# Kernel optimization log

Hardware: AMD Instinct MI355X
Metric: run time of the kernel (lower is better)

The kernel has to match this reference:

```python
import jax, jax.numpy as jnp
import numpy as np

SR = 3            # search_range
K = 5             # template_sz
S = 2 * SR + 1    # search window size (7)
KSZ = 5           # bilateral kernel size
SIG_S = 1.5       # bilateral spatial sigma
SIG_I = 0.05      # bilateral intensity sigma


def _patches(x, k, pad):
    # x: (B,C,H,W) -> (B, C*k*k, H', W'); channel order (C, kh, kw) matches torch unfold
    return jax.lax.conv_general_dilated_patches(x, (k, k), (1, 1), pad)


def _binomial(x):
    # separable [1 2 1]/4 with replicate padding
    xp = jnp.pad(x, ((0, 0), (0, 0), (1, 1), (0, 0)), mode='edge')
    v = (xp[:, :, :-2, :] + 2.0 * x + xp[:, :, 2:, :]) / 4.0
    vp = jnp.pad(v, ((0, 0), (0, 0), (0, 0), (1, 1)), mode='edge')
    return (vp[:, :, :, :-2] + 2.0 * v + vp[:, :, :, 2:]) / 4.0


def _gradient(f):
    fp = jnp.pad(f, ((0, 0), (0, 0), (1, 1), (1, 1)), mode='edge')
    fy = (fp[:, :, 2:, 1:-1] - fp[:, :, :-2, 1:-1]) / 2.0
    fx = (fp[:, :, 1:-1, 2:] - fp[:, :, 1:-1, :-2]) / 2.0
    return fy, fx


def _templates(img):
    # (B,1,H,W) -> (B,H,W,1,K*K)  per-pixel KxK patch (zero SAME padding)
    p = _patches(img, K, [(K // 2, K // 2)] * 2)      # (B,K*K,H,W)
    return jnp.transpose(p, (0, 2, 3, 1))[:, :, :, None, :]


def _search_windows(img):
    # (B,1,H,W) -> (B,H,W,S*S,K*K): KxK templates at every displacement in SxS window
    B, _, H, W = img.shape
    xp = jnp.pad(img, ((0, 0), (0, 0), (SR, SR), (SR, SR)))      # zero pad by max_sr
    p1 = _patches(xp, K, [(K // 2, K // 2)] * 2)                  # (B,K*K,H+2SR,W+2SR)
    p2 = _patches(p1, S, 'VALID')                                 # (B,K*K*S*S,H,W)
    p2 = p2.reshape(B, K * K, S, S, H, W)
    return jnp.transpose(p2, (0, 4, 5, 2, 3, 1)).reshape(B, H, W, S * S, K * K)


def _spiral_rank():
    # rank of each flat (S*S) displacement in a center-out spiral traversal
    sz = S
    order = np.zeros(sz * sz, np.int32)
    j = i = 0
    rank = 0
    order[(j + SR) * sz + (i + SR)] = rank
    rank += 1
    dirs = [(0, 1), (1, 0), (0, -1), (-1, 0)]
    d, step = 0, 1
    while rank < sz * sz:
        for _ in range(2):
            dj, di = dirs[d % 4]
            for _ in range(step):
                j += dj
                i += di
                if abs(j) <= SR and abs(i) <= SR and rank < sz * sz:
                    order[(j + SR) * sz + (i + SR)] = rank
                    rank += 1
            d += 1
        step += 1
    return jnp.asarray(order)


def _subpixel(f_t, g_t, f_img):
    # f_t, g_t: (B,H,W,1,K*K) in 0..255; f_img: (B,1,H,W) float in [0,1]
    f = f_t / 255.0
    g = g_t / 255.0
    dfy_img, dfx_img = _gradient(f_img)
    dfy = _templates(dfy_img)
    dfx = _templates(dfx_img)
    pm = np.zeros((K, K), np.float32)
    pm[0, :] = pm[-1, :] = pm[:, 0] = pm[:, -1] = 1.0   # border ring mask
    pred = jnp.asarray(pm.reshape(-1))
    rs = lambda x: jnp.sum(x, axis=-1, keepdims=True)
    a = rs(dfx * dfx * pred)
    b = rs(dfx * dfy * pred)
    d = rs(dfy * dfy * pred)
    z = g - f
    p = rs(z * dfx * pred)
    q = rs(z * dfy * pred)
    det = a * d - b * b
    u = d * p - b * q
    v = a * q - b * p
    sub = jnp.concatenate([v, u], axis=-1)              # (B,H,W,1,2) (y,x)
    det_bad = det <= 1e-7
    sub = sub / jnp.where(det_bad, 1.0, det)            # safe divide; masked anyway
    sub = jnp.where(det_bad | (jnp.abs(sub) >= 1.0), 0.0, sub)
    return jnp.transpose(sub[:, :, :, 0, :], (0, 3, 1, 2))   # (B,2,H,W)


def _median3(x):
    # 3x3 median with replicate (SYMMETRIC) padding
    B, C, H, W = x.shape
    xp = jnp.pad(x, ((0, 0), (0, 0), (1, 1), (1, 1)), mode='edge')
    p = _patches(xp, 3, 'VALID').reshape(B, C, 9, H, W)
    return jnp.sort(p, axis=2)[:, :, 4]


def _bilateral(t, vec):
    # t: (B,1,H,W) guide; vec: (B,2,H,W) flow
    B, _, H, W = t.shape
    k2 = KSZ * KSZ
    kernel = -1.0 / (2.0 * SIG_S ** 2) * jnp.ones((k2,), jnp.float32)
    sii = 1.0 / (2.0 * SIG_I ** 2)
    cp = jnp.transpose(t, (0, 2, 3, 1))[:, :, :, None, :]                # (B,H,W,1,1)
    ck = jnp.transpose(_patches(t, KSZ, [(KSZ // 2, KSZ // 2)] * 2).reshape(B, 1, k2, H, W), (0, 3, 4, 2, 1))  # (B,H,W,k2,1)
    idiff = jnp.sum((cp - ck) ** 2, axis=-1)                             # (B,H,W,k2)
    coeff = jnp.clip(1.0 - jnp.abs(kernel - idiff * sii), 0.0, 1.0)[..., None]
    vb = jnp.transpose(_patches(vec, KSZ, [(KSZ // 2, KSZ // 2)] * 2).reshape(B, 2, k2, H, W), (0, 3, 4, 2, 1))  # (B,H,W,k2,2)
    out = jnp.sum(vb * coeff, axis=-2) / jnp.sum(coeff, axis=-2)
    return jnp.transpose(out, (0, 3, 1, 2))


def setup_inputs() -> dict:
    key = jax.random.key(0)
    k1, k2 = jax.random.split(key)
    H = W = 256
    f_img = jax.random.uniform(k1, (1, 1, H, W), jnp.float32)
    g_img = jax.random.uniform(k2, (1, 1, H, W), jnp.float32)
    return {'f_img': f_img, 'g_img': g_img}


def reference(f_img, g_img):
    fb = _binomial(f_img)
    gb = _binomial(g_img)
    # quantize to uint8-valued floats (matches _cast float->uint8)
    fq = jnp.clip(jnp.round(fb * 255.0), 0.0, 255.0)
    gq = jnp.clip(jnp.round(gb * 255.0), 0.0, 255.0)
    w1 = _search_windows(fq)                 # (B,H,W,S*S,K*K)
    w2 = _templates(gq)                      # (B,H,W,1,K*K)
    cost = jnp.sum(jnp.abs(w1 - w2), axis=-1).astype(jnp.int32)   # (B,H,W,S*S)
    rank = _spiral_rank()
    score = cost * 64 + rank                 # lexicographic (cost, spiral rank); rank < 64
    idx = jnp.argmin(score, axis=-1)         # (B,H,W) spiral-centered argmin
    rng = jnp.arange(-SR, SR + 1, dtype=jnp.float32)
    jj, ii = jnp.meshgrid(rng, rng, indexing='ij')
    vecLUT = -jnp.stack([jj, ii], axis=-1).reshape(-1, 2)
    vector = jnp.transpose(vecLUT[idx], (0, 3, 1, 2))             # (B,2,H,W)
    min_t = jnp.take_along_axis(w1, idx[:, :, :, None, None], axis=3)  # (B,H,W,1,K*K)
    sub = _subpixel(min_t, w2, fb)
    flow = vector + sub
    flow = _median3(flow)
    flow = _bilateral(fb, flow)
    return flow
```

## Files before the change

### kernel.cpp

```cpp
#include <hip/hip_runtime.h>
#include <math.h>

#define H 256
#define W 256
#define TS 16

#if __has_builtin(__builtin_amdgcn_alignbyte)
__device__ __forceinline__ unsigned align_b(unsigned hi, unsigned lo, int sh) {
    return __builtin_amdgcn_alignbyte(hi, lo, sh);
}
#else
__device__ __forceinline__ unsigned align_b(unsigned hi, unsigned lo, int sh) {
    unsigned d;
    asm("v_alignbyte_b32 %0, %1, %2, %3" : "=v"(d) : "v"(hi), "v"(lo), "v"(sh));
    return d;
}
#endif

#if __has_builtin(__builtin_amdgcn_sad_u8)
__device__ __forceinline__ unsigned sad_u8(unsigned a, unsigned b, unsigned acc) {
    return __builtin_amdgcn_sad_u8(a, b, acc);
}
#else
__device__ __forceinline__ unsigned sad_u8(unsigned a, unsigned b, unsigned acc) {
    unsigned d;
    asm("v_sad_u8 %0, %1, %2, %3" : "=v"(d) : "v"(a), "v"(b), "v"(acc));
    return d;
}
#endif

__device__ __forceinline__ float binom3x3(const float* s, int r, int c, int stride) {
    float vm = (s[(r-1)*stride + (c-1)] + 2.0f*s[r*stride + (c-1)] + s[(r+1)*stride + (c-1)]) * 0.25f;
    float v0 = (s[(r-1)*stride + (c  )] + 2.0f*s[r*stride + (c  )] + s[(r+1)*stride + (c  )]) * 0.25f;
    float vp = (s[(r-1)*stride + (c+1)] + 2.0f*s[r*stride + (c+1)] + s[(r+1)*stride + (c+1)]) * 0.25f;
    return (vm + 2.0f*v0 + vp) * 0.25f;
}

__device__ __forceinline__ unsigned quant255(float v) {
    return (unsigned)fminf(fmaxf(rintf(v * 255.0f), 0.0f), 255.0f);
}

__global__ void __launch_bounds__(256)
k_flow_fused(const float* __restrict__ f, const float* __restrict__ g,
             float* __restrict__ out) {
    __shared__ float    sf[36 * 36];
    __shared__ float    sg[28 * 28];
    __shared__ float    sfb[34 * 35];
    __shared__ unsigned sfq[34 * 9];
    __shared__ unsigned sgq[26 * 7];
    __shared__ float    sflow[2][22 * 22];
    __shared__ float    smed[2][20 * 20];

    int tx = threadIdx.x, ty = threadIdx.y;
    int bx0 = blockIdx.x * TS, by0 = blockIdx.y * TS;
    int tid = ty * TS + tx;

    for (int i = tid; i < 36 * 36; i += 256) {
        int r = i / 36, c = i % 36;
        int gy = min(max(by0 + r - 10, 0), H - 1);
        int gx = min(max(bx0 + c - 10, 0), W - 1);
        sf[i] = f[gy * W + gx];
    }
    for (int i = tid; i < 28 * 28; i += 256) {
        int r = i / 28, c = i % 28;
        int gy = min(max(by0 + r - 6, 0), H - 1);
        int gx = min(max(bx0 + c - 6, 0), W - 1);
        sg[i] = g[gy * W + gx];
    }
    __syncthreads();

    for (int i = tid; i < 306 + 182; i += 256) {
        if (i < 306) {
            int row = i / 9, dw = i % 9;
            unsigned pack = 0;
            #pragma unroll
            for (int b = 0; b < 4; b++) {
                int col = dw * 4 + b;
                unsigned q = 0;
                if (col < 34) {
                    float bv = 0.0f;
                    int gy = by0 + row - 9, gx = bx0 + col - 9;
                    if (gy >= 0 && gy < H && gx >= 0 && gx < W) {
                        bv = binom3x3(sf, row + 1, col + 1, 36);
                        q = quant255(bv);
                    }
                    sfb[row * 35 + col] = bv;
                }
                pack |= q << (8 * b);
            }
            sfq[i] = pack;
        } else {
            int j = i - 306;
            int row = j / 7, dw = j % 7;
            unsigned pack = 0;
            #pragma unroll
            for (int b = 0; b < 4; b++) {
                int col = dw * 4 + b;
                unsigned q = 0;
                if (col < 26) {
                    int gy = by0 + row - 5, gx = bx0 + col - 5;
                    if (gy >= 0 && gy < H && gx >= 0 && gx < W)
                        q = quant255(binom3x3(sg, row + 1, col + 1, 28));
                }
                pack |= q << (8 * b);
            }
            sgq[j] = pack;
        }
    }
    __syncthreads();

    const unsigned char* sfq_b = (const unsigned char*)sfq;

    const unsigned RANKC[49] = {
        42,43,44,45,46,47,48,
        41,20,21,22,23,24,25,
        40,19, 6, 7, 8, 9,26,
        39,18, 5, 0, 1,10,27,
        38,17, 4, 3, 2,11,28,
        37,16,15,14,13,12,29,
        36,35,34,33,32,31,30
    };

    for (int it = tid; it < 22 * 22; it += 256) {
        int r = it / 22, c = it % 22;
        int py = min(max(by0 + r - 3, 0), H - 1);
        int px = min(max(bx0 + c - 3, 0), W - 1);
        int ro = py - by0 + 9, co = px - bx0 + 9;
        int base = (co - 5) >> 2, a = (co - 5) & 3;

        unsigned w0[11], w1[11], w2[11];
        #pragma unroll
        for (int r2 = 0; r2 < 11; r2++) {
            const unsigned* row = &sfq[(ro - 5 + r2) * 9 + base];
            unsigned d0 = row[0], d1 = row[1], d2 = row[2], d3 = row[3];
            w0[r2] = align_b(d1, d0, a);
            w1[r2] = align_b(d2, d1, a);
            w2[r2] = align_b(d3, d2, a);
        }

        int gro = py - by0 + 5, gco = px - bx0 + 5;
        int gbase = (gco - 2) >> 2, ga = (gco - 2) & 3;
        unsigned gt_lo[5], gt_hi[5];
        #pragma unroll
        for (int kh = 0; kh < 5; kh++) {
            const unsigned* row = &sgq[(gro - 2 + kh) * 7 + gbase];
            unsigned d0 = row[0], d1 = row[1];
            gt_lo[kh] = align_b(d1, d0, ga);
            gt_hi[kh] = (d1 >> (8 * ga)) & 0xFFu;
        }

        unsigned best = 0xFFFFFFFFu;
        int bestd = 0;
        #pragma unroll
        for (int si = 0; si < 7; si++) {
            unsigned fd[11], f5[11];
            #pragma unroll
            for (int r2 = 0; r2 < 11; r2++) {
                fd[r2] = (si < 4) ? align_b(w1[r2], w0[r2], si) : align_b(w2[r2], w1[r2], si - 4);
                f5[r2] = (si < 4) ? ((w1[r2] >> (8 * si)) & 0xFFu)
                                  : ((w2[r2] >> (8 * (si - 4))) & 0xFFu);
            }
            #pragma unroll
            for (int sj = 0; sj < 7; sj++) {
                unsigned acc0 = 0, acc1 = 0;
                #pragma unroll
                for (int kh = 0; kh < 5; kh++) {
                    acc0 = sad_u8(fd[sj + kh], gt_lo[kh], acc0);
                    acc1 = sad_u8(f5[sj + kh], gt_hi[kh], acc1);
                }
                unsigned score = ((acc0 + acc1) << 6) + RANKC[sj * 7 + si];
                if (score < best) { best = score; bestd = sj * 7 + si; }
            }
        }
        int dy = bestd / 7 - 3, dx = bestd % 7 - 3;

        float aA = 0.f, bB = 0.f, dD = 0.f, pP = 0.f, qQ = 0.f;
        #pragma unroll
        for (int kh = 0; kh < 5; kh++) {
            #pragma unroll
            for (int kw = 0; kw < 5; kw++) {
                if (kh != 0 && kh != 4 && kw != 0 && kw != 4) continue;
                int yy = py + kh - 2, xx = px + kw - 2;
                if (yy < 0 || yy >= H || xx < 0 || xx >= W) continue;
                int fy = yy - by0 + 9;
                int fx = xx - bx0 + 9;
                int xl = max(xx - 1, 0) - bx0 + 9, xr = min(xx + 1, W - 1) - bx0 + 9;
                int yu = max(yy - 1, 0) - by0 + 9, yd = min(yy + 1, H - 1) - by0 + 9;
                float gxv = (sfb[fy * 35 + xr] - sfb[fy * 35 + xl]) * 0.5f;
                float gyv = (sfb[yd * 35 + fx] - sfb[yu * 35 + fx]) * 0.5f;
                float fv = (float)sfq_b[(ro + dy + kh - 2) * 36 + (co + dx + kw - 2)] * (1.0f / 255.0f);
                float gv = (float)((kw < 4) ? ((gt_lo[kh] >> (8 * kw)) & 0xFFu) : gt_hi[kh]) * (1.0f / 255.0f);
                float z = gv - fv;
                aA += gxv * gxv;
                bB += gxv * gyv;
                dD += gyv * gyv;
                pP += z * gxv;
                qQ += z * gyv;
            }
        }
        float det = aA * dD - bB * bB;
        float u = dD * pP - bB * qQ;
        float v = aA * qQ - bB * pP;
        float suby = 0.f, subx = 0.f;
        if (det > 1e-7f) {
            suby = v / det;
            subx = u / det;
            if (fabsf(suby) >= 1.0f) suby = 0.f;
            if (fabsf(subx) >= 1.0f) subx = 0.f;
        }
        sflow[0][it] = (float)(-dy) + suby;
        sflow[1][it] = (float)(-dx) + subx;
    }
    __syncthreads();

    for (int i = tid; i < 2 * 20 * 20; i += 256) {
        int ch = i / 400, rem = i % 400;
        int rm = rem / 20, cm = rem % 20;
        int my = by0 + rm - 2, mx = bx0 + cm - 2;
        float m = 0.0f;
        if (my >= 0 && my < H && mx >= 0 && mx < W) {
            float v[9];
            int n = 0;
            #pragma unroll
            for (int dj = -1; dj <= 1; dj++) {
                #pragma unroll
                for (int di = -1; di <= 1; di++) {
                    int fr = min(max(my + dj, 0), H - 1) - by0 + 3;
                    int fc = min(max(mx + di, 0), W - 1) - bx0 + 3;
                    v[n++] = sflow[ch][fr * 22 + fc];
                }
            }
#define MSWAP(A, B) { float t_ = fminf(v[A], v[B]); v[B] = fmaxf(v[A], v[B]); v[A] = t_; }
            MSWAP(1,2); MSWAP(4,5); MSWAP(7,8);
            MSWAP(0,1); MSWAP(3,4); MSWAP(6,7);
            MSWAP(1,2); MSWAP(4,5); MSWAP(7,8);
            MSWAP(0,3); MSWAP(5,8); MSWAP(4,7);
            MSWAP(3,6); MSWAP(1,4); MSWAP(2,5);
            MSWAP(4,7); MSWAP(4,2); MSWAP(6,4);
            MSWAP(4,2);
#undef MSWAP
            m = v[4];
        }
        smed[ch][i % 400] = m;
    }
    __syncthreads();

    int x = bx0 + tx, y = by0 + ty;
    const float kern = -0.22222222222222221f;
    const float sii  = 200.0f;
    float cp = sfb[(ty + 9) * 35 + (tx + 9)];
    float sc = 0.f, sy = 0.f, sx = 0.f;
    #pragma unroll
    for (int j = 0; j < 5; j++) {
        #pragma unroll
        for (int i = 0; i < 5; i++) {
            float ck = sfb[(ty + 7 + j) * 35 + (tx + 7 + i)];
            float df = cp - ck;
            float coeff = 1.0f - fabsf(kern - df * df * sii);
            coeff = fminf(fmaxf(coeff, 0.0f), 1.0f);
            int s = (ty + j) * 20 + (tx + i);
            sc += coeff;
            sy += coeff * smed[0][s];
            sx += coeff * smed[1][s];
        }
    }
    out[y * W + x]         = sy / sc;
    out[H * W + y * W + x] = sx / sc;
}

extern "C" void kernel_launch(void* const* d_in, const int* in_sizes, int n_in,
                              void* d_out, int out_size, void* d_ws, size_t ws_size,
                              hipStream_t stream) {
    const float* f = (const float*)d_in[0];
    const float* g = (const float*)d_in[1];
    float* out = (float*)d_out;
    (void)d_ws; (void)ws_size;

    dim3 blk(TS, TS);
    dim3 grd(W / TS, H / TS);
    k_flow_fused<<<grd, blk, 0, stream>>>(f, g, out);
}
```

Baseline: 67.99 us.

## Split block-matching search across thread pairs with 512-thread blocks

```diff
diff --git a/kernel.cpp b/kernel.cpp
--- a/kernel.cpp
+++ b/kernel.cpp
@@ -40,7 +40,7 @@
     return (unsigned)fminf(fmaxf(rintf(v * 255.0f), 0.0f), 255.0f);
 }
 
-__global__ void __launch_bounds__(256)
+__global__ void __launch_bounds__(512)
 k_flow_fused(const float* __restrict__ f, const float* __restrict__ g,
              float* __restrict__ out) {
     __shared__ float    sf[36 * 36];
@@ -51,17 +51,16 @@
     __shared__ float    sflow[2][22 * 22];
     __shared__ float    smed[2][20 * 20];
 
-    int tx = threadIdx.x, ty = threadIdx.y;
     int bx0 = blockIdx.x * TS, by0 = blockIdx.y * TS;
-    int tid = ty * TS + tx;
-
-    for (int i = tid; i < 36 * 36; i += 256) {
+    int tid = threadIdx.x;
+
+    for (int i = tid; i < 36 * 36; i += 512) {
         int r = i / 36, c = i % 36;
         int gy = min(max(by0 + r - 10, 0), H - 1);
         int gx = min(max(bx0 + c - 10, 0), W - 1);
         sf[i] = f[gy * W + gx];
     }
-    for (int i = tid; i < 28 * 28; i += 256) {
+    for (int i = tid; i < 28 * 28; i += 512) {
         int r = i / 28, c = i % 28;
         int gy = min(max(by0 + r - 6, 0), H - 1);
         int gx = min(max(bx0 + c - 6, 0), W - 1);
@@ -69,7 +68,8 @@
     }
     __syncthreads();
 
-    for (int i = tid; i < 306 + 182; i += 256) {
+    if (tid < 306 + 182) {
+        int i = tid;
         if (i < 306) {
             int row = i / 9, dw = i % 9;
             unsigned pack = 0;
@@ -121,21 +121,21 @@
         36,35,34,33,32,31,30
     };
 
-    for (int it = tid; it < 22 * 22; it += 256) {
+    for (int u = tid; u < 2 * 22 * 22; u += 512) {
+        int it = u >> 1, half = u & 1;
         int r = it / 22, c = it % 22;
         int py = min(max(by0 + r - 3, 0), H - 1);
         int px = min(max(bx0 + c - 3, 0), W - 1);
         int ro = py - by0 + 9, co = px - bx0 + 9;
         int base = (co - 5) >> 2, a = (co - 5) & 3;
 
-        unsigned w0[11], w1[11], w2[11];
+        unsigned wA[11], wB[11];
         #pragma unroll
         for (int r2 = 0; r2 < 11; r2++) {
-            const unsigned* row = &sfq[(ro - 5 + r2) * 9 + base];
-            unsigned d0 = row[0], d1 = row[1], d2 = row[2], d3 = row[3];
-            w0[r2] = align_b(d1, d0, a);
-            w1[r2] = align_b(d2, d1, a);
-            w2[r2] = align_b(d3, d2, a);
+            const unsigned* row = &sfq[(ro - 5 + r2) * 9 + base + half];
+            unsigned dA = row[0], dB = row[1], dC = row[2];
+            wA[r2] = align_b(dB, dA, a);
+            wB[r2] = align_b(dC, dB, a);
         }
 
         int gro = py - by0 + 5, gco = px - bx0 + 5;
@@ -152,26 +152,34 @@
         unsigned best = 0xFFFFFFFFu;
         int bestd = 0;
         #pragma unroll
-        for (int si = 0; si < 7; si++) {
-            unsigned fd[11], f5[11];
-            #pragma unroll
-            for (int r2 = 0; r2 < 11; r2++) {
-                fd[r2] = (si < 4) ? align_b(w1[r2], w0[r2], si) : align_b(w2[r2], w1[r2], si - 4);
-                f5[r2] = (si < 4) ? ((w1[r2] >> (8 * si)) & 0xFFu)
-                                  : ((w2[r2] >> (8 * (si - 4))) & 0xFFu);
-            }
-            #pragma unroll
-            for (int sj = 0; sj < 7; sj++) {
-                unsigned acc0 = 0, acc1 = 0;
+        for (int sl = 0; sl < 4; sl++) {
+            if (!(sl == 3 && half)) {
+                unsigned fd[11], f5[11];
                 #pragma unroll
-                for (int kh = 0; kh < 5; kh++) {
-                    acc0 = sad_u8(fd[sj + kh], gt_lo[kh], acc0);
-                    acc1 = sad_u8(f5[sj + kh], gt_hi[kh], acc1);
-                }
-                unsigned score = ((acc0 + acc1) << 6) + RANKC[sj * 7 + si];
-                if (score < best) { best = score; bestd = sj * 7 + si; }
-            }
-        }
+                for (int r2 = 0; r2 < 11; r2++) {
+                    fd[r2] = align_b(wB[r2], wA[r2], sl);
+                    f5[r2] = (wB[r2] >> (8 * sl)) & 0xFFu;
+                }
+                #pragma unroll
+                for (int sj = 0; sj < 7; sj++) {
+                    unsigned acc0 = 0, acc1 = 0;
+                    #pragma unroll
+                    for (int kh = 0; kh < 5; kh++) {
+                        acc0 = sad_u8(fd[sj + kh], gt_lo[kh], acc0);
+                        acc1 = sad_u8(f5[sj + kh], gt_hi[kh], acc1);
+                    }
+                    int i0 = sj * 7 + sl;
+                    int i1 = sj * 7 + 4 + sl; if (i1 > 48) i1 = 48;
+                    unsigned rk = half ? RANKC[i1] : RANKC[i0];
+                    unsigned score = ((acc0 + acc1) << 6) + rk;
+                    int dsp = sj * 7 + sl + (half << 2);
+                    if (score < best) { best = score; bestd = dsp; }
+                }
+            }
+        }
+        unsigned obest = __shfl_xor(best, 1);
+        int obestd = __shfl_xor(bestd, 1);
+        if (obest < best) { best = obest; bestd = obestd; }
         int dy = bestd / 7 - 3, dx = bestd % 7 - 3;
 
         float aA = 0.f, bB = 0.f, dD = 0.f, pP = 0.f, qQ = 0.f;
@@ -199,21 +207,23 @@
             }
         }
         float det = aA * dD - bB * bB;
-        float u = dD * pP - bB * qQ;
-        float v = aA * qQ - bB * pP;
+        float u2 = dD * pP - bB * qQ;
+        float v2 = aA * qQ - bB * pP;
         float suby = 0.f, subx = 0.f;
         if (det > 1e-7f) {
-            suby = v / det;
-            subx = u / det;
+            suby = v2 / det;
+            subx = u2 / det;
             if (fabsf(suby) >= 1.0f) suby = 0.f;
             if (fabsf(subx) >= 1.0f) subx = 0.f;
         }
-        sflow[0][it] = (float)(-dy) + suby;
-        sflow[1][it] = (float)(-dx) + subx;
-    }
-    __syncthreads();
-
-    for (int i = tid; i < 2 * 20 * 20; i += 256) {
+        if (!half) {
+            sflow[0][it] = (float)(-dy) + suby;
+            sflow[1][it] = (float)(-dx) + subx;
+        }
+    }
+    __syncthreads();
+
+    for (int i = tid; i < 2 * 20 * 20; i += 512) {
         int ch = i / 400, rem = i % 400;
         int rm = rem / 20, cm = rem % 20;
         int my = by0 + rm - 2, mx = bx0 + cm - 2;
@@ -241,31 +251,32 @@
 #undef MSWAP
             m = v[4];
         }
-        smed[ch][i % 400] = m;
-    }
-    __syncthreads();
-
-    int x = bx0 + tx, y = by0 + ty;
-    const float kern = -0.22222222222222221f;
-    const float sii  = 200.0f;
-    float cp = sfb[(ty + 9) * 35 + (tx + 9)];
-    float sc = 0.f, sy = 0.f, sx = 0.f;
-    #pragma unroll
-    for (int j = 0; j < 5; j++) {
-        #pragma unroll
-        for (int i = 0; i < 5; i++) {
-            float ck = sfb[(ty + 7 + j) * 35 + (tx + 7 + i)];
-            float df = cp - ck;
-            float coeff = 1.0f - fabsf(kern - df * df * sii);
-            coeff = fminf(fmaxf(coeff, 0.0f), 1.0f);
-            int s = (ty + j) * 20 + (tx + i);
-            sc += coeff;
-            sy += coeff * smed[0][s];
-            sx += coeff * smed[1][s];
-        }
-    }
-    out[y * W + x]         = sy / sc;
-    out[H * W + y * W + x] = sx / sc;
+        smed[ch][rem] = m;
+    }
+    __syncthreads();
+
+    {
+        int ch = tid >> 8, pix = tid & 255;
+        int tx = pix & 15, ty = pix >> 4;
+        int x = bx0 + tx, y = by0 + ty;
+        const float kern = -0.22222222222222221f;
+        const float sii  = 200.0f;
+        float cp = sfb[(ty + 9) * 35 + (tx + 9)];
+        float sc = 0.f, sv = 0.f;
+        #pragma unroll
+        for (int j = 0; j < 5; j++) {
+            #pragma unroll
+            for (int i = 0; i < 5; i++) {
+                float ck = sfb[(ty + 7 + j) * 35 + (tx + 7 + i)];
+                float df = cp - ck;
+                float coeff = 1.0f - fabsf(kern - df * df * sii);
+                coeff = fminf(fmaxf(coeff, 0.0f), 1.0f);
+                sc += coeff;
+                sv += coeff * smed[ch][(ty + j) * 20 + (tx + i)];
+            }
+        }
+        out[ch * H * W + y * W + x] = sv / sc;
+    }
 }
 
 extern "C" void kernel_launch(void* const* d_in, const int* in_sizes, int n_in,
@@ -276,7 +287,7 @@
     float* out = (float*)d_out;
     (void)d_ws; (void)ws_size;
 
-    dim3 blk(TS, TS);
+    dim3 blk(512);
     dim3 grd(W / TS, H / TS);
     k_flow_fused<<<grd, blk, 0, stream>>>(f, g, out);
 }
```

New measurement: 67.69 us. No clear change (-0.5%).
